# Kernel tuning notes

Measured on AMD Instinct MI355X. Metric: run time of the kernel, lower is better.

## Reference

```python
import jax, jax.numpy as jnp
import numpy as np

K = 3          # s_kernel_size = max_graph_distance + 1
C_OUT = 128    # out_channel


def setup_inputs() -> dict:
    key = jax.random.key(0)
    k1, k2, k3, k4 = jax.random.split(key, 4)
    N, C_IN, T, V = 64, 64, 256, 25
    x = jax.random.normal(k1, (N, C_IN, T, V), dtype=jnp.float32)
    # 1x1 Conv2d(in_channel, out_channel*K) weight/bias
    W = jax.random.normal(k2, (K * C_OUT, C_IN), dtype=jnp.float32) * 0.05
    b = jax.random.normal(k3, (K * C_OUT,), dtype=jnp.float32) * 0.05
    # fixed adjacency stack (non-trainable buffer-like param)
    A = jax.random.uniform(k4, (K, V, V), dtype=jnp.float32)
    edge = jnp.ones((K, V, V), dtype=jnp.float32)       # init ones_like(A)
    adaptive_A = jnp.zeros((K, V, V), dtype=jnp.float32)  # init zeros_like(A)
    return {"x": x, "W": W, "b": b, "A": A, "edge": edge, "adaptive_A": adaptive_A}


def reference(x, W, b, A, edge, adaptive_A):
    n, c_in, t, v = x.shape
    # 1x1 conv == per-pixel GEMM over channel dim: (n,c,t,v) -> (n, K*C_OUT, t, v)
    y = jnp.einsum('nctv,oc->notv', x, W) + b[None, :, None, None]
    y = y.reshape(n, K, C_OUT, t, v)                 # (n, k, c, t, v)
    effective_A = A * edge + adaptive_A              # (k, v, w)
    out = jnp.einsum('nkctv,kvw->nctw', y, effective_A)
    return out
```

## Files before the change

kernel.cpp:

```cpp
#include <hip/hip_runtime.h>
#include <hip/hip_bf16.h>

typedef __bf16 bf16x8 __attribute__((ext_vector_type(8)));
typedef __bf16 bf16x4 __attribute__((ext_vector_type(4)));
typedef float floatx4 __attribute__((ext_vector_type(4)));
typedef float floatx4u __attribute__((ext_vector_type(4), aligned(4)));

#define ROWK 200
#define ZROWS 112

__global__ void sgc_prep(const float* __restrict__ W, const float* __restrict__ b,
                         const float* __restrict__ A, const float* __restrict__ edge,
                         const float* __restrict__ adA,
                         __hip_bfloat16* __restrict__ Wp, __hip_bfloat16* __restrict__ effAB,
                         float* __restrict__ bias2) {
  int tid = blockIdx.x * blockDim.x + threadIdx.x;
  int nthr = gridDim.x * blockDim.x;
  for (int i = tid; i < 24576; i += nthr) {
    int c = i / 192; int r = i - c * 192; int k = r >> 6; int ci = r & 63;
    Wp[i] = __float2bfloat16(W[(k * 128 + c) * 64 + ci]);
  }
  for (int i = tid; i < 2560; i += nthr) {
    int n = i >> 5; int v = i & 31;
    float val = 0.f;
    if (n < 75 && v < 25) {
      int k = n / 25; int w = n - k * 25;
      int idx = (k * 25 + v) * 25 + w;
      val = A[idx] * edge[idx] + adA[idx];
    }
    effAB[i] = __float2bfloat16(val);
  }
  for (int i = tid; i < 3200; i += nthr) {
    int c = i / 25; int w = i - c * 25;
    float s = 0.f;
    for (int k = 0; k < 3; k++) {
      float sv = 0.f;
      for (int v = 0; v < 25; v++) {
        int idx = (k * 25 + v) * 25 + w;
        sv += A[idx] * edge[idx] + adA[idx];
      }
      s += b[k * 128 + c] * sv;
    }
    bias2[i] = s;
  }
}

__global__ __launch_bounds__(256, 3)
void sgc_main(const float* __restrict__ x,
              const __hip_bfloat16* __restrict__ Wp,
              const __hip_bfloat16* __restrict__ effAB,
              const float* __restrict__ bias2,
              float* __restrict__ out) {
  __shared__ __hip_bfloat16 zt[ZROWS * ROWK];
  const int tid = threadIdx.x;
  const int lane = tid & 63;
  const int wv = tid >> 6;
  const int blk = blockIdx.x;

  const int col = lane & 15;
  const int quad = lane >> 4;
  const int kb = quad * 8;

  bf16x8 bA[5];
#pragma unroll
  for (int nt = 0; nt < 5; nt++)
    bA[nt] = *(const bf16x8*)(effAB + (nt * 16 + col) * 32 + kb);

  {
    const int g = blk * 4 + wv;
    const int n0 = g >> 8, t = g & 255;
    const float* xbase = x + (size_t)(n0 * 64) * 6400 + (size_t)t * 25;
#pragma unroll
    for (int mt = 0; mt < 4; mt++) {
      const int ci = mt * 16 + col;
      const float* xr = xbase + (size_t)ci * 6400;
      bf16x8 xa;
      if (quad < 3) {
        floatx4u a = *(const floatx4u*)(xr + kb);
        floatx4u c = *(const floatx4u*)(xr + kb + 4);
        xa = (bf16x8){(__bf16)a.x, (__bf16)a.y, (__bf16)a.z, (__bf16)a.w,
                      (__bf16)c.x, (__bf16)c.y, (__bf16)c.z, (__bf16)c.w};
      } else {
        float v24 = xr[24];
        xa = (bf16x8){(__bf16)v24, (__bf16)0.f, (__bf16)0.f, (__bf16)0.f,
                      (__bf16)0.f, (__bf16)0.f, (__bf16)0.f, (__bf16)0.f};
      }
      floatx4 zacc[5];
#pragma unroll
      for (int nt = 0; nt < 5; nt++) {
        zacc[nt] = (floatx4){0.f, 0.f, 0.f, 0.f};
        zacc[nt] = __builtin_amdgcn_mfma_f32_16x16x32_bf16(xa, bA[nt], zacc[nt], 0, 0, 0);
      }
#pragma unroll
      for (int nt = 0; nt < 5; nt++) {
        int nn = nt * 16 + col;
        if (nn < 75) {
          int k = (nn * 41) >> 10;
          int w = nn - k * 25;
          bf16x4 zb = (bf16x4){(__bf16)zacc[nt][0], (__bf16)zacc[nt][1],
                               (__bf16)zacc[nt][2], (__bf16)zacc[nt][3]};
          *(bf16x4*)(zt + (wv * 25 + w) * ROWK + k * 64 + mt * 16 + quad * 4) = zb;
        }
      }
    }
  }

  bf16x8 afr[2][6];
#pragma unroll
  for (int mtl = 0; mtl < 2; mtl++) {
    int c = (2 * wv + mtl) * 16 + col;
    const __hip_bfloat16* wrow = Wp + c * 192;
#pragma unroll
    for (int ks = 0; ks < 6; ks++)
      afr[mtl][ks] = *(const bf16x8*)(wrow + ks * 32 + kb);
  }

  floatx4 acc[2][7];
#pragma unroll
  for (int nt = 0; nt < 7; nt++) {
    int nn = nt * 16 + col;
    int p = (nn * 41) >> 10;
    int w = nn - p * 25;
#pragma unroll
    for (int mtl = 0; mtl < 2; mtl++) {
      int c0 = (2 * wv + mtl) * 16 + quad * 4;
#pragma unroll
      for (int r = 0; r < 4; r++)
        acc[mtl][nt][r] = bias2[(c0 + r) * 25 + w];
    }
  }

  __syncthreads();

  const __hip_bfloat16* ztp = zt;
#pragma unroll
  for (int ks = 0; ks < 6; ks++) {
    bf16x8 bfr[7];
#pragma unroll
    for (int nt = 0; nt < 7; nt++)
      bfr[nt] = *(const bf16x8*)(ztp + (nt * 16 + col) * ROWK + ks * 32 + kb);
#pragma unroll
    for (int nt = 0; nt < 7; nt++) {
      acc[0][nt] = __builtin_amdgcn_mfma_f32_16x16x32_bf16(afr[0][ks], bfr[nt], acc[0][nt], 0, 0, 0);
      acc[1][nt] = __builtin_amdgcn_mfma_f32_16x16x32_bf16(afr[1][ks], bfr[nt], acc[1][nt], 0, 0, 0);
    }
  }

#pragma unroll
  for (int nt = 0; nt < 7; nt++) {
    int nn = nt * 16 + col;
    if (nn >= 100) continue;
    int p = (nn * 41) >> 10;
    int w = nn - p * 25;
    int g = blk * 4 + p;
    int n = g >> 8, t = g & 255;
#pragma unroll
    for (int mtl = 0; mtl < 2; mtl++) {
      int c0 = (2 * wv + mtl) * 16 + quad * 4;
      size_t base = ((size_t)(n * 128 + c0) * 256 + t) * 25 + w;
#pragma unroll
      for (int r = 0; r < 4; r++)
        out[base + (size_t)r * 6400] = acc[mtl][nt][r];
    }
  }
}

extern "C" void kernel_launch(void* const* d_in, const int* in_sizes, int n_in,
                              void* d_out, int out_size, void* d_ws, size_t ws_size,
                              hipStream_t stream) {
  const float* x    = (const float*)d_in[0];
  const float* W    = (const float*)d_in[1];
  const float* b    = (const float*)d_in[2];
  const float* A    = (const float*)d_in[3];
  const float* edge = (const float*)d_in[4];
  const float* adA  = (const float*)d_in[5];
  float* out = (float*)d_out;

  char* ws = (char*)d_ws;
  __hip_bfloat16* Wp    = (__hip_bfloat16*)ws;
  __hip_bfloat16* effAB = (__hip_bfloat16*)(ws + 49152);
  float* bias2          = (float*)(ws + 54272);

  sgc_prep<<<64, 256, 0, stream>>>(W, b, A, edge, adA, Wp, effAB, bias2);
  sgc_main<<<4096, 256, 0, stream>>>(x, Wp, effAB, bias2, out);
}
```

Baseline: 378.5 us.

## Stage x loads and output stores through LDS for coalesced 16-byte global access

The block now loads its 4 contiguous timesteps of x for all input channels with coalesced float4 reads, transposes them into shared memory, and builds the MFMA A-fragments from there. Outputs are staged through shared memory too, so each channel's 100 contiguous floats are written with float4 stores instead of scattered scalar stores. The bias table is transposed so each lane's bias initialisation is one vector load, and block indices are swizzled across the batch. This costs extra shared-memory traffic and several more barriers, but is meant to relieve the global-memory access inefficiency of a bandwidth-bound kernel.

```diff
diff --git a/kernel.cpp b/kernel.cpp
--- a/kernel.cpp
+++ b/kernel.cpp
@@ -7,13 +7,13 @@
 typedef float floatx4u __attribute__((ext_vector_type(4), aligned(4)));
 
 #define ROWK 200
-#define ZROWS 112
+#define ZROWS 100
 
 __global__ void sgc_prep(const float* __restrict__ W, const float* __restrict__ b,
                          const float* __restrict__ A, const float* __restrict__ edge,
                          const float* __restrict__ adA,
                          __hip_bfloat16* __restrict__ Wp, __hip_bfloat16* __restrict__ effAB,
-                         float* __restrict__ bias2) {
+                         float* __restrict__ bias2T) {
   int tid = blockIdx.x * blockDim.x + threadIdx.x;
   int nthr = gridDim.x * blockDim.x;
   for (int i = tid; i < 24576; i += nthr) {
@@ -31,7 +31,7 @@
     effAB[i] = __float2bfloat16(val);
   }
   for (int i = tid; i < 3200; i += nthr) {
-    int c = i / 25; int w = i - c * 25;
+    int w = i >> 7; int c = i & 127;
     float s = 0.f;
     for (int k = 0; k < 3; k++) {
       float sv = 0.f;
@@ -41,7 +41,7 @@
       }
       s += b[k * 128 + c] * sv;
     }
-    bias2[i] = s;
+    bias2T[i] = s;
   }
 }
 
@@ -49,59 +49,32 @@
 void sgc_main(const float* __restrict__ x,
               const __hip_bfloat16* __restrict__ Wp,
               const __hip_bfloat16* __restrict__ effAB,
-              const float* __restrict__ bias2,
+              const float* __restrict__ bias2T,
               float* __restrict__ out) {
-  __shared__ __hip_bfloat16 zt[ZROWS * ROWK];
+  __shared__ __hip_bfloat16 lds[ZROWS * ROWK];
+  __hip_bfloat16* zt = lds;
+  float* xs = (float*)lds;
+  float* eb = (float*)lds;
+
   const int tid = threadIdx.x;
   const int lane = tid & 63;
   const int wv = tid >> 6;
-  const int blk = blockIdx.x;
-
+  const int blk0 = blockIdx.x;
+  const int blk = (blk0 & 7) * 512 + (blk0 >> 3);
   const int col = lane & 15;
   const int quad = lane >> 4;
   const int kb = quad * 8;
-
-  bf16x8 bA[5];
-#pragma unroll
-  for (int nt = 0; nt < 5; nt++)
-    bA[nt] = *(const bf16x8*)(effAB + (nt * 16 + col) * 32 + kb);
-
-  {
-    const int g = blk * 4 + wv;
-    const int n0 = g >> 8, t = g & 255;
-    const float* xbase = x + (size_t)(n0 * 64) * 6400 + (size_t)t * 25;
-#pragma unroll
-    for (int mt = 0; mt < 4; mt++) {
-      const int ci = mt * 16 + col;
-      const float* xr = xbase + (size_t)ci * 6400;
-      bf16x8 xa;
-      if (quad < 3) {
-        floatx4u a = *(const floatx4u*)(xr + kb);
-        floatx4u c = *(const floatx4u*)(xr + kb + 4);
-        xa = (bf16x8){(__bf16)a.x, (__bf16)a.y, (__bf16)a.z, (__bf16)a.w,
-                      (__bf16)c.x, (__bf16)c.y, (__bf16)c.z, (__bf16)c.w};
-      } else {
-        float v24 = xr[24];
-        xa = (bf16x8){(__bf16)v24, (__bf16)0.f, (__bf16)0.f, (__bf16)0.f,
-                      (__bf16)0.f, (__bf16)0.f, (__bf16)0.f, (__bf16)0.f};
-      }
-      floatx4 zacc[5];
-#pragma unroll
-      for (int nt = 0; nt < 5; nt++) {
-        zacc[nt] = (floatx4){0.f, 0.f, 0.f, 0.f};
-        zacc[nt] = __builtin_amdgcn_mfma_f32_16x16x32_bf16(xa, bA[nt], zacc[nt], 0, 0, 0);
-      }
-#pragma unroll
-      for (int nt = 0; nt < 5; nt++) {
-        int nn = nt * 16 + col;
-        if (nn < 75) {
-          int k = (nn * 41) >> 10;
-          int w = nn - k * 25;
-          bf16x4 zb = (bf16x4){(__bf16)zacc[nt][0], (__bf16)zacc[nt][1],
-                               (__bf16)zacc[nt][2], (__bf16)zacc[nt][3]};
-          *(bf16x4*)(zt + (wv * 25 + w) * ROWK + k * 64 + mt * 16 + quad * 4) = zb;
-        }
-      }
+  const int g0 = blk * 4;
+  const int n = g0 >> 8, t0 = g0 & 255;
+
+  floatx4 xr[7];
+  const float* xn = x + (size_t)n * 64 * 6400 + t0 * 25;
+#pragma unroll
+  for (int i = 0; i < 7; i++) {
+    int f = tid + 256 * i;
+    if (f < 1600) {
+      int ci = f / 25, q = f - ci * 25;
+      xr[i] = *(const floatx4u*)(xn + (size_t)ci * 6400 + q * 4);
     }
   }
 
@@ -113,6 +86,26 @@
 #pragma unroll
     for (int ks = 0; ks < 6; ks++)
       afr[mtl][ks] = *(const bf16x8*)(wrow + ks * 32 + kb);
+  }
+
+  bf16x8 bA[5];
+#pragma unroll
+  for (int nt = 0; nt < 5; nt++)
+    bA[nt] = *(const bf16x8*)(effAB + (nt * 16 + col) * 32 + kb);
+
+#pragma unroll
+  for (int i = 0; i < 7; i++) {
+    int f = tid + 256 * i;
+    if (f < 1600) {
+      int ci = f / 25;
+      int q4 = (f - ci * 25) * 4;
+#pragma unroll
+      for (int e = 0; e < 4; e++) {
+        int rr = q4 + e;
+        int tt = rr / 25, v = rr - tt * 25;
+        xs[(tt * 64 + ci) * 28 + v] = xr[i][e];
+      }
+    }
   }
 
   floatx4 acc[2][7];
@@ -124,21 +117,68 @@
 #pragma unroll
     for (int mtl = 0; mtl < 2; mtl++) {
       int c0 = (2 * wv + mtl) * 16 + quad * 4;
-#pragma unroll
-      for (int r = 0; r < 4; r++)
-        acc[mtl][nt][r] = bias2[(c0 + r) * 25 + w];
-    }
-  }
-
-  __syncthreads();
-
-  const __hip_bfloat16* ztp = zt;
+      acc[mtl][nt] = *(const floatx4*)(bias2T + w * 128 + c0);
+    }
+  }
+
+  __syncthreads();
+
+  bf16x8 xa[4];
+#pragma unroll
+  for (int mt = 0; mt < 4; mt++) {
+    int ci = mt * 16 + col;
+    const float* base = xs + (wv * 64 + ci) * 28;
+    if (quad < 3) {
+      floatx4 a = *(const floatx4*)(base + kb);
+      floatx4 c = *(const floatx4*)(base + kb + 4);
+      xa[mt] = (bf16x8){(__bf16)a.x, (__bf16)a.y, (__bf16)a.z, (__bf16)a.w,
+                        (__bf16)c.x, (__bf16)c.y, (__bf16)c.z, (__bf16)c.w};
+    } else {
+      float v24 = base[24];
+      xa[mt] = (bf16x8){(__bf16)v24, (__bf16)0.f, (__bf16)0.f, (__bf16)0.f,
+                        (__bf16)0.f, (__bf16)0.f, (__bf16)0.f, (__bf16)0.f};
+    }
+  }
+
+  __syncthreads();
+
+#pragma unroll
+  for (int mt = 0; mt < 4; mt++) {
+    floatx4 zacc[5];
+#pragma unroll
+    for (int nt = 0; nt < 5; nt++) {
+      zacc[nt] = (floatx4){0.f, 0.f, 0.f, 0.f};
+      zacc[nt] = __builtin_amdgcn_mfma_f32_16x16x32_bf16(xa[mt], bA[nt], zacc[nt], 0, 0, 0);
+    }
+#pragma unroll
+    for (int nt = 0; nt < 5; nt++) {
+      int nn = nt * 16 + col;
+      if (nn < 75) {
+        int k = (nn * 41) >> 10;
+        int w = nn - k * 25;
+        bf16x4 zb = (bf16x4){(__bf16)zacc[nt][0], (__bf16)zacc[nt][1],
+                             (__bf16)zacc[nt][2], (__bf16)zacc[nt][3]};
+        *(bf16x4*)(zt + (wv * 25 + w) * ROWK + k * 64 + mt * 16 + quad * 4) = zb;
+      }
+    }
+  }
+
+  int zoff[7];
+#pragma unroll
+  for (int nt = 0; nt < 7; nt++) {
+    int nn = nt * 16 + col;
+    int rr = (nt == 6) ? (nn < 100 ? nn : 99) : nn;
+    zoff[nt] = rr * ROWK + kb;
+  }
+
+  __syncthreads();
+
 #pragma unroll
   for (int ks = 0; ks < 6; ks++) {
     bf16x8 bfr[7];
 #pragma unroll
     for (int nt = 0; nt < 7; nt++)
-      bfr[nt] = *(const bf16x8*)(ztp + (nt * 16 + col) * ROWK + ks * 32 + kb);
+      bfr[nt] = *(const bf16x8*)(zt + zoff[nt] + ks * 32);
 #pragma unroll
     for (int nt = 0; nt < 7; nt++) {
       acc[0][nt] = __builtin_amdgcn_mfma_f32_16x16x32_bf16(afr[0][ks], bfr[nt], acc[0][nt], 0, 0, 0);
@@ -146,22 +186,33 @@
     }
   }
 
-#pragma unroll
-  for (int nt = 0; nt < 7; nt++) {
-    int nn = nt * 16 + col;
-    if (nn >= 100) continue;
-    int p = (nn * 41) >> 10;
-    int w = nn - p * 25;
-    int g = blk * 4 + p;
-    int n = g >> 8, t = g & 255;
-#pragma unroll
-    for (int mtl = 0; mtl < 2; mtl++) {
-      int c0 = (2 * wv + mtl) * 16 + quad * 4;
-      size_t base = ((size_t)(n * 128 + c0) * 256 + t) * 25 + w;
-#pragma unroll
-      for (int r = 0; r < 4; r++)
-        out[base + (size_t)r * 6400] = acc[mtl][nt][r];
-    }
+  __syncthreads();
+
+#pragma unroll
+  for (int h = 0; h < 2; h++) {
+    int slotbase = wv * 16 + quad * 4;
+#pragma unroll
+    for (int nt = 0; nt < 7; nt++) {
+      int nn = nt * 16 + col;
+      if (nn < 100) {
+#pragma unroll
+        for (int r = 0; r < 4; r++)
+          eb[(slotbase + r) * 100 + nn] = acc[h][nt][r];
+      }
+    }
+    __syncthreads();
+#pragma unroll
+    for (int i = 0; i < 7; i++) {
+      int f = tid + 256 * i;
+      if (f < 1600) {
+        int slot = f / 25, q = f - slot * 25;
+        floatx4 v = *(const floatx4*)(eb + slot * 100 + q * 4);
+        int c = 32 * (slot >> 4) + 16 * h + (slot & 15);
+        float* ob = out + ((size_t)(n * 128 + c) * 256 + t0) * 25 + q * 4;
+        *(floatx4u*)ob = v;
+      }
+    }
+    __syncthreads();
   }
 }
 
@@ -179,8 +230,8 @@
   char* ws = (char*)d_ws;
   __hip_bfloat16* Wp    = (__hip_bfloat16*)ws;
   __hip_bfloat16* effAB = (__hip_bfloat16*)(ws + 49152);
-  float* bias2          = (float*)(ws + 54272);
-
-  sgc_prep<<<64, 256, 0, stream>>>(W, b, A, edge, adA, Wp, effAB, bias2);
-  sgc_main<<<4096, 256, 0, stream>>>(x, Wp, effAB, bias2, out);
+  float* bias2T         = (float*)(ws + 54272);
+
+  sgc_prep<<<64, 256, 0, stream>>>(W, b, A, edge, adA, Wp, effAB, bias2T);
+  sgc_main<<<4096, 256, 0, stream>>>(x, Wp, effAB, bias2T, out);
 }
```

Result: faster. 363.4 us (-4.0%).
